# Kernel tuning notes

Measured on AMD Instinct MI355X. Metric: run time of the kernel, lower is better.

The kernel has to match this reference:

```python
import jax, jax.numpy as jnp
import numpy as np

B, N, C, K, COUT = 2, 16384, 64, 17, 128  # K = neighbors+self; kernel_size = K-1


def setup_inputs() -> dict:
    key = jax.random.key(0)
    kx, ka, kw = jax.random.split(key, 3)
    x = jax.random.normal(kx, (B, N, C), dtype=jnp.float32)
    # neighbor indices in [0, N), guaranteed != self via offset trick (avoids 0/0 in frame normalization)
    off = jax.random.randint(ka, (B, N, K), 1, N)
    adj = ((jnp.arange(N)[None, :, None] + off) % N).astype(jnp.int32)
    # kaiming_uniform-like init scale
    bound = 1.0 / np.sqrt(C * (K - 1))
    weight = jax.random.uniform(kw, (COUT, C, K - 1), dtype=jnp.float32, minval=-bound, maxval=bound)
    return {"x": x, "adj": adj, "weight": weight}


def reference(x, adj, weight):
    # x: [B,N,C], adj: [B,N,K] int, weight: [Cout,C,K-1]
    knn_idx = adj[:, :, 1:]                      # [B,N,K-1] drop self column
    knn = jax.vmap(lambda xb, ib: xb[ib])(x, knn_idx)   # gather -> [B,N,K-1,C]
    diff = knn - x[:, :, None, :]                # [B,N,K-1,C]
    norm = jnp.sqrt(jnp.sum(diff * diff, axis=-1, keepdims=True))   # [B,N,K-1,1]
    frame = jnp.concatenate([diff, norm], axis=-1)                  # [B,N,K-1,C+1]
    frame = frame / jnp.sqrt(jnp.sum(frame * frame, axis=-1, keepdims=True))
    radius = 1.0
    proj = radius * frame[..., :-1]              # drop norm coord -> [B,N,K-1,C]
    # per-neighbor kernel slice contraction, then ReLU and max over neighborhood
    out = jnp.einsum('ocj,bnjc->bonj', weight, proj)  # [B,Cout,N,K-1]
    out = jnp.max(jax.nn.relu(out), axis=-1)          # [B,Cout,N]
    return out
```

## Files before the change

### kernel.cpp

```cpp
#include <hip/hip_runtime.h>
#include <hip/hip_bf16.h>

typedef __attribute__((ext_vector_type(8))) short bf16x8;
typedef __attribute__((ext_vector_type(4))) float f32x4;

#define N_PTS   16384
#define C_CH    64
#define K_ADJ   17
#define C_OUT   128
#define N_J     16

__device__ __hip_bfloat16 g_wb[N_J * C_OUT * C_CH];

__global__ __launch_bounds__(256) void prep_weights_k(const float* __restrict__ w) {
    int idx = blockIdx.x * 256 + threadIdx.x;
    int S   = idx >> 3, r = idx & 7;
    int c   = S >> 12, s = S & 4095;
    int row = s >> 3,  c8 = s & 7;
    int p8  = c8 ^ (row & 7);
    int j   = c * 4 + (row >> 7);
    int o   = row & 127;
    int p   = p8 * 8 + r;
    int hi  = p >> 5, q = p & 31, la = q >> 3, rr = q & 7;
    int ch  = hi * 32 + (rr < 4 ? la * 4 + rr : 16 + la * 4 + (rr - 4));
    g_wb[idx] = __float2bfloat16(w[(o * C_CH + ch) * (K_ADJ - 1) + j]);
}

#define GLOAD(gp, lp) __builtin_amdgcn_global_load_lds(                       \
    (const __attribute__((address_space(1))) void*)(gp),                      \
    (__attribute__((address_space(3))) void*)(lp), 16, 0, 0)

struct PF { float4 v0, v1, v2, v3; };

__device__ __forceinline__ void issue_gather(PF& p, const float* __restrict__ xb,
                                             int row, int lk) {
    const float* gp = xb + (size_t)row * C_CH + lk * 4;
    p.v0 = *(const float4*)(gp +  0);
    p.v1 = *(const float4*)(gp + 16);
    p.v2 = *(const float4*)(gp + 32);
    p.v3 = *(const float4*)(gp + 48);
}

__global__ __launch_bounds__(512, 2) void sconv_k(
    const float* __restrict__ x,
    const int*   __restrict__ adj,
    float*       __restrict__ out)
{
    __shared__ __hip_bfloat16 lds_w[2][4 * C_OUT * C_CH];

    const int pblk = blockIdx.x;
    const int g8   = pblk & 7;
    const int b    = g8 >> 2;
    const int slot = ((pblk >> 3) << 2) | (g8 & 3);

    const int tid  = threadIdx.x;
    const int lane = tid & 63;
    const int w8   = tid >> 6;
    const int lrow = lane & 15;
    const int lk   = lane >> 4;

    const int n = slot * 128 + w8 * 16 + lrow;

    const float* __restrict__ xb   = x   + (size_t)b * N_PTS * C_CH;
    const int*   __restrict__ adjb = adj + (size_t)b * N_PTS * K_ADJ;
    float*       __restrict__ ob   = out + (size_t)b * C_OUT * N_PTS;

    #pragma unroll
    for (int i = 0; i < 8; ++i) {
        const int lo = (w8 * 8 + i) * 512;
        GLOAD(g_wb +         lo + lane * 8, &lds_w[0][lo]);
        GLOAD(g_wb + 32768 + lo + lane * 8, &lds_w[1][lo]);
    }

    float ctr[16];
    {
        const float* rp = xb + (size_t)n * C_CH + lk * 4;
        #pragma unroll
        for (int i = 0; i < 4; ++i) {
            float4 v = *(const float4*)(rp + i * 16);
            ctr[i*4+0]=v.x; ctr[i*4+1]=v.y; ctr[i*4+2]=v.z; ctr[i*4+3]=v.w;
        }
    }

    int aidx[N_J];
    {
        const int base = n * K_ADJ + 1;
        #pragma unroll
        for (int j = 0; j < N_J; ++j) aidx[j] = adjb[base + j];
    }

    f32x4 maxacc[8];
    #pragma unroll
    for (int of = 0; of < 8; ++of) maxacc[of] = f32x4{0.f, 0.f, 0.f, 0.f};

    PF pf0, pf1;
    issue_gather(pf0, xb, aidx[0], lk);
    issue_gather(pf1, xb, aidx[1], lk);

    __syncthreads();

    const int sw = lrow & 7;

    #pragma unroll
    for (int c = 0; c < 4; ++c) {
        const __hip_bfloat16* buf = lds_w[c & 1];

        #pragma unroll
        for (int jj = 0; jj < 4; ++jj) {
            const int j = c * 4 + jj;

            float d[16];
            {
                const PF& p = (j & 1) ? pf1 : pf0;
                d[0] =p.v0.x; d[1] =p.v0.y; d[2] =p.v0.z; d[3] =p.v0.w;
                d[4] =p.v1.x; d[5] =p.v1.y; d[6] =p.v1.z; d[7] =p.v1.w;
                d[8] =p.v2.x; d[9] =p.v2.y; d[10]=p.v2.z; d[11]=p.v2.w;
                d[12]=p.v3.x; d[13]=p.v3.y; d[14]=p.v3.z; d[15]=p.v3.w;
            }
            if (j + 2 < N_J) {
                if (j & 1) issue_gather(pf1, xb, aidx[j + 2], lk);
                else       issue_gather(pf0, xb, aidx[j + 2], lk);
            }

            float s = 0.f;
            #pragma unroll
            for (int i = 0; i < 16; ++i) { d[i] -= ctr[i]; s = fmaf(d[i], d[i], s); }
            s += __shfl_xor(s, 16);
            s += __shfl_xor(s, 32);
            const float scale = rsqrtf(2.0f * s);

            bf16x8 bf0, bf1;
            #pragma unroll
            for (int i = 0; i < 8; ++i) {
                bf0[i] = (short)__builtin_bit_cast(unsigned short, __float2bfloat16(d[i]     * scale));
                bf1[i] = (short)__builtin_bit_cast(unsigned short, __float2bfloat16(d[i + 8] * scale));
            }

            #pragma unroll
            for (int of = 0; of < 8; ++of) {
                const int row = jj * 128 + of * 16 + lrow;
                const bf16x8 a0 = *(const bf16x8*)&buf[(row * 8 + ( lk      ^ sw)) * 8];
                const bf16x8 a1 = *(const bf16x8*)&buf[(row * 8 + ((4 + lk) ^ sw)) * 8];
                f32x4 acc = f32x4{0.f, 0.f, 0.f, 0.f};
                acc = __builtin_amdgcn_mfma_f32_16x16x32_bf16(a0, bf0, acc, 0, 0, 0);
                acc = __builtin_amdgcn_mfma_f32_16x16x32_bf16(a1, bf1, acc, 0, 0, 0);
                #pragma unroll
                for (int r = 0; r < 4; ++r)
                    maxacc[of][r] = fmaxf(maxacc[of][r], acc[r]);
            }
        }

        __syncthreads();
        if (c < 2) {
            #pragma unroll
            for (int i = 0; i < 8; ++i) {
                const int lo = (w8 * 8 + i) * 512;
                GLOAD(g_wb + (c + 2) * 32768 + lo + lane * 8, &lds_w[c & 1][lo]);
            }
        }
    }

    #pragma unroll
    for (int of = 0; of < 8; ++of) {
        const int o0 = of * 16 + lk * 4;
        #pragma unroll
        for (int r = 0; r < 4; ++r)
            ob[(size_t)(o0 + r) * N_PTS + n] = maxacc[of][r];
    }
}

extern "C" void kernel_launch(void* const* d_in, const int* in_sizes, int n_in,
                              void* d_out, int out_size, void* d_ws, size_t ws_size,
                              hipStream_t stream) {
    (void)in_sizes; (void)n_in; (void)d_ws; (void)ws_size; (void)out_size;
    const float* x   = (const float*)d_in[0];
    const int*   adj = (const int*)d_in[1];
    const float* w   = (const float*)d_in[2];
    float*       out = (float*)d_out;

    hipLaunchKernelGGL(prep_weights_k, dim3(512), dim3(256), 0, stream, w);
    hipLaunchKernelGGL(sconv_k,        dim3(256), dim3(512), 0, stream, x, adj, out);
}
```

Baseline: 89.11 us.

## Pre-convert x to bf16 so neighbor gathers move half the bytes

A new pre-pass kernel converts x to bf16 and stores it in a global buffer. The main kernel then gathers 16-byte contiguous bf16 chunks per lane, which changes the per-lane channel mapping, so the weight packing is simplified to match. Gather traffic is halved and the loads are wider, at the cost of an extra launch and a full pass over x. Differences and norms are now computed from bf16-rounded inputs, which reduces accuracy.

```diff
diff --git a/kernel.cpp b/kernel.cpp
--- a/kernel.cpp
+++ b/kernel.cpp
@@ -10,9 +10,27 @@
 #define C_OUT   128
 #define N_J     16
 
-__device__ __hip_bfloat16 g_wb[N_J * C_OUT * C_CH];
-
-__global__ __launch_bounds__(256) void prep_weights_k(const float* __restrict__ w) {
+__device__ __align__(16) __hip_bfloat16 g_xb[2 * N_PTS * C_CH];
+
+__device__ __align__(16) __hip_bfloat16 g_wb[N_J * C_OUT * C_CH];
+
+__global__ __launch_bounds__(256) void prep_x_k(const float* __restrict__ x) {
+    int t = blockIdx.x * 256 + threadIdx.x;
+    const float4 v0 = *(const float4*)(x + t * 8);
+    const float4 v1 = *(const float4*)(x + t * 8 + 4);
+    bf16x8 o;
+    o[0] = (short)__builtin_bit_cast(unsigned short, __float2bfloat16(v0.x));
+    o[1] = (short)__builtin_bit_cast(unsigned short, __float2bfloat16(v0.y));
+    o[2] = (short)__builtin_bit_cast(unsigned short, __float2bfloat16(v0.z));
+    o[3] = (short)__builtin_bit_cast(unsigned short, __float2bfloat16(v0.w));
+    o[4] = (short)__builtin_bit_cast(unsigned short, __float2bfloat16(v1.x));
+    o[5] = (short)__builtin_bit_cast(unsigned short, __float2bfloat16(v1.y));
+    o[6] = (short)__builtin_bit_cast(unsigned short, __float2bfloat16(v1.z));
+    o[7] = (short)__builtin_bit_cast(unsigned short, __float2bfloat16(v1.w));
+    *(bf16x8*)&g_xb[t * 8] = o;
+}
+
+__global__ __launch_bounds__(256) void prep_w_k(const float* __restrict__ w) {
     int idx = blockIdx.x * 256 + threadIdx.x;
     int S   = idx >> 3, r = idx & 7;
     int c   = S >> 12, s = S & 4095;
@@ -20,9 +38,7 @@
     int p8  = c8 ^ (row & 7);
     int j   = c * 4 + (row >> 7);
     int o   = row & 127;
-    int p   = p8 * 8 + r;
-    int hi  = p >> 5, q = p & 31, la = q >> 3, rr = q & 7;
-    int ch  = hi * 32 + (rr < 4 ? la * 4 + rr : 16 + la * 4 + (rr - 4));
+    int ch  = p8 * 8 + r;
     g_wb[idx] = __float2bfloat16(w[(o * C_CH + ch) * (K_ADJ - 1) + j]);
 }
 
@@ -30,21 +46,18 @@
     (const __attribute__((address_space(1))) void*)(gp),                      \
     (__attribute__((address_space(3))) void*)(lp), 16, 0, 0)
 
-struct PF { float4 v0, v1, v2, v3; };
-
-__device__ __forceinline__ void issue_gather(PF& p, const float* __restrict__ xb,
+struct PFB { bf16x8 u0, u1; };
+
+__device__ __forceinline__ void issue_gather(PFB& p, const __hip_bfloat16* __restrict__ xbb,
                                              int row, int lk) {
-    const float* gp = xb + (size_t)row * C_CH + lk * 4;
-    p.v0 = *(const float4*)(gp +  0);
-    p.v1 = *(const float4*)(gp + 16);
-    p.v2 = *(const float4*)(gp + 32);
-    p.v3 = *(const float4*)(gp + 48);
+    const __hip_bfloat16* gp = xbb + row * C_CH + lk * 8;
+    p.u0 = *(const bf16x8*)(gp);
+    p.u1 = *(const bf16x8*)(gp + 32);
 }
 
 __global__ __launch_bounds__(512, 2) void sconv_k(
-    const float* __restrict__ x,
-    const int*   __restrict__ adj,
-    float*       __restrict__ out)
+    const int* __restrict__ adj,
+    float*     __restrict__ out)
 {
     __shared__ __hip_bfloat16 lds_w[2][4 * C_OUT * C_CH];
 
@@ -61,9 +74,9 @@
 
     const int n = slot * 128 + w8 * 16 + lrow;
 
-    const float* __restrict__ xb   = x   + (size_t)b * N_PTS * C_CH;
-    const int*   __restrict__ adjb = adj + (size_t)b * N_PTS * K_ADJ;
-    float*       __restrict__ ob   = out + (size_t)b * C_OUT * N_PTS;
+    const __hip_bfloat16* __restrict__ xbb = g_xb + b * (N_PTS * C_CH);
+    const int* __restrict__ adjb = adj + (size_t)b * N_PTS * K_ADJ;
+    float*     __restrict__ ob   = out + (size_t)b * C_OUT * N_PTS;
 
     #pragma unroll
     for (int i = 0; i < 8; ++i) {
@@ -74,11 +87,13 @@
 
     float ctr[16];
     {
-        const float* rp = xb + (size_t)n * C_CH + lk * 4;
-        #pragma unroll
-        for (int i = 0; i < 4; ++i) {
-            float4 v = *(const float4*)(rp + i * 16);
-            ctr[i*4+0]=v.x; ctr[i*4+1]=v.y; ctr[i*4+2]=v.z; ctr[i*4+3]=v.w;
+        const __hip_bfloat16* cp = xbb + n * C_CH + lk * 8;
+        const bf16x8 c0 = *(const bf16x8*)(cp);
+        const bf16x8 c1 = *(const bf16x8*)(cp + 32);
+        #pragma unroll
+        for (int i = 0; i < 8; ++i) {
+            ctr[i]     = __bfloat162float(__builtin_bit_cast(__hip_bfloat16, (unsigned short)c0[i]));
+            ctr[i + 8] = __bfloat162float(__builtin_bit_cast(__hip_bfloat16, (unsigned short)c1[i]));
         }
     }
 
@@ -93,9 +108,9 @@
     #pragma unroll
     for (int of = 0; of < 8; ++of) maxacc[of] = f32x4{0.f, 0.f, 0.f, 0.f};
 
-    PF pf0, pf1;
-    issue_gather(pf0, xb, aidx[0], lk);
-    issue_gather(pf1, xb, aidx[1], lk);
+    PFB pf0, pf1;
+    issue_gather(pf0, xbb, aidx[0], lk);
+    issue_gather(pf1, xbb, aidx[1], lk);
 
     __syncthreads();
 
@@ -111,20 +126,21 @@
 
             float d[16];
             {
-                const PF& p = (j & 1) ? pf1 : pf0;
-                d[0] =p.v0.x; d[1] =p.v0.y; d[2] =p.v0.z; d[3] =p.v0.w;
-                d[4] =p.v1.x; d[5] =p.v1.y; d[6] =p.v1.z; d[7] =p.v1.w;
-                d[8] =p.v2.x; d[9] =p.v2.y; d[10]=p.v2.z; d[11]=p.v2.w;
-                d[12]=p.v3.x; d[13]=p.v3.y; d[14]=p.v3.z; d[15]=p.v3.w;
+                const PFB& p = (j & 1) ? pf1 : pf0;
+                #pragma unroll
+                for (int i = 0; i < 8; ++i) {
+                    d[i]     = __bfloat162float(__builtin_bit_cast(__hip_bfloat16, (unsigned short)p.u0[i])) - ctr[i];
+                    d[i + 8] = __bfloat162float(__builtin_bit_cast(__hip_bfloat16, (unsigned short)p.u1[i])) - ctr[i + 8];
+                }
             }
             if (j + 2 < N_J) {
-                if (j & 1) issue_gather(pf1, xb, aidx[j + 2], lk);
-                else       issue_gather(pf0, xb, aidx[j + 2], lk);
+                if (j & 1) issue_gather(pf1, xbb, aidx[j + 2], lk);
+                else       issue_gather(pf0, xbb, aidx[j + 2], lk);
             }
 
             float s = 0.f;
             #pragma unroll
-            for (int i = 0; i < 16; ++i) { d[i] -= ctr[i]; s = fmaf(d[i], d[i], s); }
+            for (int i = 0; i < 16; ++i) s = fmaf(d[i], d[i], s);
             s += __shfl_xor(s, 16);
             s += __shfl_xor(s, 32);
             const float scale = rsqrtf(2.0f * s);
@@ -178,6 +194,7 @@
     const float* w   = (const float*)d_in[2];
     float*       out = (float*)d_out;
 
-    hipLaunchKernelGGL(prep_weights_k, dim3(512), dim3(256), 0, stream, w);
-    hipLaunchKernelGGL(sconv_k,        dim3(256), dim3(512), 0, stream, x, adj, out);
-}
+    hipLaunchKernelGGL(prep_x_k, dim3(1024), dim3(256), 0, stream, x);
+    hipLaunchKernelGGL(prep_w_k, dim3(512),  dim3(256), 0, stream, w);
+    hipLaunchKernelGGL(sconv_k,  dim3(256),  dim3(512), 0, stream, adj, out);
+}
```

After: 83.09 us. 6.8% less time.
